# Kernel optimization log

Hardware: AMD Instinct MI355X
Metric: run time of the kernel (lower is better)

## Reference

```python
import jax, jax.numpy as jnp
import numpy as np

E4M3_MAX = 448.0  # max finite value of float8_e4m3fn
TILE = 64


def tile_quant_dequant(x):
    # per-row 1x64 tile quantization: scale = amax(tile)/448, fp8 e4m3 round-trip
    M, K = x.shape
    xt = x.reshape(M, K // TILE, TILE)
    amax = jnp.max(jnp.abs(xt), axis=-1, keepdims=True)
    scale = jnp.maximum(amax, 1e-12) / E4M3_MAX
    q = (xt / scale).astype(jnp.float8_e4m3fn).astype(jnp.float32)
    return (q * scale).reshape(M, K)


def block_quant_dequant(w):
    # 64x64 block quantization of the weight matrix
    N, K = w.shape
    wb = w.reshape(N // TILE, TILE, K // TILE, TILE)
    amax = jnp.max(jnp.abs(wb), axis=(1, 3), keepdims=True)
    scale = jnp.maximum(amax, 1e-12) / E4M3_MAX
    q = (wb / scale).astype(jnp.float8_e4m3fn).astype(jnp.float32)
    return (q * scale).reshape(N, K)


def setup_inputs() -> dict:
    key = jax.random.key(0)
    k1, k2 = jax.random.split(key)
    B, S, K, N = 2, 4096, 4096, 4096
    x = jax.random.normal(k1, (B, S, K), dtype=jnp.float32)
    # kaiming_uniform_(a=sqrt(5)) on [N,K] -> U(-1/sqrt(K), 1/sqrt(K))
    bound = float(1.0 / np.sqrt(K))
    weight = jax.random.uniform(k2, (N, K), jnp.float32, -bound, bound)
    bias = jnp.zeros((N,), jnp.float32)
    return {"x": x, "weight": weight, "bias": bias}


def reference(x, weight, bias):
    N, K = weight.shape
    x2d = x.reshape(-1, K)                     # [M, K]
    xq = tile_quant_dequant(x2d)               # simulated fp8 tile-quantized input
    wq = block_quant_dequant(weight)           # simulated fp8 block-quantized weight
    # fp8 GEMM with scales == matmul of dequantized operands (fp32 accumulation),
    # low-precision output then fp32 bias add (bf16 + fp32 bias -> fp32 in torch)
    out = jnp.matmul(xq, wq.T).astype(jnp.bfloat16).astype(jnp.float32)
    out = out + bias
    return out.reshape(*x.shape[:-1], N)
```

## Files before the change

### kernel.cpp

```cpp
#include <hip/hip_runtime.h>

typedef __attribute__((ext_vector_type(4))) float f32x4;
typedef __attribute__((ext_vector_type(16))) float f32x16;
typedef __attribute__((ext_vector_type(4))) int i32x4;
typedef __attribute__((ext_vector_type(8))) int i32x8;

__device__ __forceinline__ unsigned char enc_e4m3(float y) {
    unsigned int u = __float_as_uint(y);
    unsigned int s = (u >> 31) << 7;
    unsigned int a = u & 0x7fffffffu;
    if (a >= 0x3C800000u) {
        unsigned int r = a + 0x7FFFFu + ((a >> 20) & 1u);
        r &= 0xFFF00000u;
        if (r > 0x43E00000u) r = 0x43E00000u;
        unsigned int e = (r >> 23) - 120u;
        return (unsigned char)(s | (e << 3) | ((r >> 20) & 7u));
    } else {
        int m = (int)rintf(__uint_as_float(a) * 512.0f);
        return (unsigned char)(s | (unsigned)m);
    }
}

__device__ __forceinline__ unsigned short f32_to_bf16_bits(float f) {
    unsigned int u = __float_as_uint(f);
    u += 0x7FFFu + ((u >> 16) & 1u);
    return (unsigned short)(u >> 16);
}

__global__ __launch_bounds__(256) void quant_x_kernel(const float* __restrict__ x,
                                                      unsigned char* __restrict__ xq,
                                                      float* __restrict__ xsT,
                                                      long long n4, int K, int M) {
    long long g = (long long)blockIdx.x * 256 + threadIdx.x;
    if (g >= n4) return;
    f32x4 v = ((const f32x4*)x)[g];
    float a = fmaxf(fmaxf(fabsf(v.x), fabsf(v.y)), fmaxf(fabsf(v.z), fabsf(v.w)));
    a = fmaxf(a, __shfl_xor(a, 1));
    a = fmaxf(a, __shfl_xor(a, 2));
    a = fmaxf(a, __shfl_xor(a, 4));
    a = fmaxf(a, __shfl_xor(a, 8));
    float scale = fmaxf(a, 1e-12f) / 448.0f;
    long long flat = g * 4;
    uchar4 o;
    o.x = enc_e4m3(v.x / scale);
    o.y = enc_e4m3(v.y / scale);
    o.z = enc_e4m3(v.z / scale);
    o.w = enc_e4m3(v.w / scale);
    *(uchar4*)(xq + flat) = o;
    int row = (int)(flat / K);
    int rem = (int)(flat % K);
    if ((rem & 63) == 0)
        xsT[(size_t)(rem >> 6) * M + row] = scale;
}

__global__ __launch_bounds__(256) void quant_w_kernel(const float* __restrict__ w,
                                                      unsigned char* __restrict__ wq,
                                                      float* __restrict__ ws,
                                                      int N, int K) {
    const int nb = blockIdx.y, kb = blockIdx.x;
    const int KT = K >> 6;
    const int t = threadIdx.x;
    const int rgrp = t >> 4;
    const int cchk = t & 15;
    f32x4 v[4];
    float a = 0.0f;
#pragma unroll
    for (int i = 0; i < 4; ++i) {
        int row = nb * 64 + rgrp + i * 16;
        v[i] = *(const f32x4*)(w + (size_t)row * K + kb * 64 + cchk * 4);
        a = fmaxf(a, fmaxf(fmaxf(fabsf(v[i].x), fabsf(v[i].y)),
                           fmaxf(fabsf(v[i].z), fabsf(v[i].w))));
    }
#pragma unroll
    for (int off = 1; off < 64; off <<= 1) a = fmaxf(a, __shfl_xor(a, off));
    __shared__ float sm[4];
    if ((t & 63) == 0) sm[t >> 6] = a;
    __syncthreads();
    a = fmaxf(fmaxf(sm[0], sm[1]), fmaxf(sm[2], sm[3]));
    float scale = fmaxf(a, 1e-12f) / 448.0f;
#pragma unroll
    for (int i = 0; i < 4; ++i) {
        int row = nb * 64 + rgrp + i * 16;
        uchar4 o;
        o.x = enc_e4m3(v[i].x / scale);
        o.y = enc_e4m3(v[i].y / scale);
        o.z = enc_e4m3(v[i].z / scale);
        o.w = enc_e4m3(v[i].w / scale);
        *(uchar4*)(wq + (size_t)row * K + kb * 64 + cchk * 4) = o;
    }
    if (t == 0) ws[(size_t)nb * KT + kb] = scale;
}

#define GLDS(srcp, ldsp) __builtin_amdgcn_global_load_lds( \
    (__attribute__((address_space(1))) void*)(srcp),       \
    (__attribute__((address_space(3))) void*)(ldsp), 16, 0, 0)

__global__ __launch_bounds__(512, 2) void gemm_fp8(const unsigned char* __restrict__ Aq,
                                                   const unsigned char* __restrict__ Bq,
                                                   const float* __restrict__ xsT,
                                                   const float* __restrict__ wss,
                                                   const float* __restrict__ bias,
                                                   float* __restrict__ C,
                                                   int M, int N, int K) {
    __shared__ unsigned char Al[2][16384];
    __shared__ unsigned char Bl[2][16384];
    const int tid = threadIdx.x;
    const int wid = tid >> 6;
    const int lane = tid & 63;
    const int wm = wid >> 2, wn = wid & 3;
    const int l31 = lane & 31, h = lane >> 5;
    const int KT = K >> 6, NT = KT;

    const int nbx = N >> 8;
    const int nwg = (M >> 8) * nbx;
    const int bid = blockIdx.x;
    const int swz = (bid & 7) * (nwg >> 3) + (bid >> 3);
    const int tm = swz / nbx, tn = swz % nbx;

    const unsigned char* gA = Aq + (size_t)tm * 256 * K;
    const unsigned char* gB = Bq + (size_t)tn * 256 * K;

    const int gswz = (((lane & 3) ^ ((lane >> 3) & 3)) << 4);

    const int fsw = (l31 >> 1) & 3;
    const int slotLo = (2 * h) ^ fsw;
    const int oX = (wm * 128 + l31) * 64;
    const int oW = (wn * 64 + l31) * 64;
    const int oXlo = oX + slotLo * 16, oXhi = oX + (slotLo ^ 1) * 16;
    const int oWlo = oW + slotLo * 16, oWhi = oW + (slotLo ^ 1) * 16;

    const int iRow = tm * 256 + wm * 128 + l31;
    const int jbw  = tn * 4 + wn;

    const f32x16 z16 = {0.f,0.f,0.f,0.f,0.f,0.f,0.f,0.f,0.f,0.f,0.f,0.f,0.f,0.f,0.f,0.f};
    f32x16 macc[2][4];
#pragma unroll
    for (int n = 0; n < 2; ++n)
#pragma unroll
        for (int m = 0; m < 4; ++m) macc[n][m] = z16;

    i32x4 xlo[4], xhi[4], wlo[2], whi[2];
    float xsA[4], xsB[4], wsA = 0.f, wsB = 0.f, sarr[4];

    auto STG = [&](int t, int bufn) {
#pragma unroll
        for (int i = 0; i < 2; ++i) {
            int seg = wid * 2 + i;
            int row = seg * 16 + (lane >> 2);
            GLDS(gA + (size_t)row * K + (size_t)t * 64 + gswz, (char*)&Al[bufn][0] + seg * 1024);
            GLDS(gB + (size_t)row * K + (size_t)t * 64 + gswz, (char*)&Bl[bufn][0] + seg * 1024);
        }
    };

    auto RD_X = [&](int buf, int mi) {
        xlo[mi] = *(const i32x4*)(&Al[buf][oXlo + mi * 2048]);
        xhi[mi] = *(const i32x4*)(&Al[buf][oXhi + mi * 2048]);
    };
    auto RD_W = [&](int buf, int ni) {
        wlo[ni] = *(const i32x4*)(&Bl[buf][oWlo + ni * 2048]);
        whi[ni] = *(const i32x4*)(&Bl[buf][oWhi + ni * 2048]);
    };

    auto CL = [&](int ni, int mi0) {
        i32x8 wf = __builtin_shufflevector(wlo[ni], whi[ni], 0, 1, 2, 3, 4, 5, 6, 7);
#pragma unroll
        for (int q = 0; q < 2; ++q) {
            const int mi = mi0 + q;
            i32x8 xf = __builtin_shufflevector(xlo[mi], xhi[mi], 0, 1, 2, 3, 4, 5, 6, 7);
            f32x16 p = __builtin_amdgcn_mfma_scale_f32_32x32x64_f8f6f4(
                wf, xf, z16, 0, 0, 0, 0x7F7F7F7F, 0, 0x7F7F7F7F);
            macc[ni][mi] += p * sarr[mi];
        }
    };

    STG(0, 0);
#pragma unroll
    for (int m = 0; m < 4; ++m) xsA[m] = xsT[iRow + m * 32];
    wsA = wss[(size_t)jbw * KT];
    asm volatile("s_waitcnt vmcnt(0)" ::: "memory");
    asm volatile("s_barrier" ::: "memory");
    RD_W(0, 0); RD_X(0, 0); RD_X(0, 1);

    auto TILE = [&](int buf, int tnx, const float (&xsC)[4], float wsC,
                    float (&xsN)[4], float& wsN) {
        const int nb = buf ^ 1;
#pragma unroll
        for (int m = 0; m < 4; ++m) sarr[m] = xsC[m] * wsC;

        STG(tnx, nb);
#pragma unroll
        for (int m = 0; m < 4; ++m) xsN[m] = xsT[(size_t)tnx * M + iRow + m * 32];
        wsN = wss[(size_t)jbw * KT + tnx];

        RD_W(buf, 1);
        asm volatile("s_waitcnt lgkmcnt(2)" ::: "memory");
        __builtin_amdgcn_sched_barrier(0);
        __builtin_amdgcn_s_setprio(1);
        CL(0, 0);
        __builtin_amdgcn_s_setprio(0);

        RD_X(buf, 2); RD_X(buf, 3);
        asm volatile("s_waitcnt lgkmcnt(4)" ::: "memory");
        __builtin_amdgcn_sched_barrier(0);
        __builtin_amdgcn_s_setprio(1);
        CL(1, 0);
        __builtin_amdgcn_s_setprio(0);

        asm volatile("s_waitcnt lgkmcnt(0)" ::: "memory");
        __builtin_amdgcn_sched_barrier(0);
        __builtin_amdgcn_s_setprio(1);
        CL(0, 2);
        CL(1, 2);
        __builtin_amdgcn_s_setprio(0);

        asm volatile("s_waitcnt vmcnt(0)" ::: "memory");
        asm volatile("s_barrier" ::: "memory");
        RD_W(nb, 0); RD_X(nb, 0); RD_X(nb, 1);
    };

    for (int t = 0; t < NT; t += 2) {
        int t1 = t + 1;
        int t2 = (t + 2 < NT) ? (t + 2) : 0;
        TILE(0, t1, xsA, wsA, xsB, wsB);
        TILE(1, t2, xsB, wsB, xsA, wsA);
    }

    const int i0 = tm * 256 + wm * 128 + l31;
    const int jn = tn * 256 + wn * 64 + 4 * h;
#pragma unroll
    for (int ni = 0; ni < 2; ++ni) {
#pragma unroll
        for (int mi = 0; mi < 4; ++mi) {
            const int row = i0 + mi * 32;
#pragma unroll
            for (int q = 0; q < 4; ++q) {
                const int col = jn + ni * 32 + 8 * q;
                f32x4 bv = *(const f32x4*)(bias + col);
                f32x4 vo;
#pragma unroll
                for (int j = 0; j < 4; ++j) {
                    unsigned short b = f32_to_bf16_bits(macc[ni][mi][q * 4 + j]);
                    vo[j] = __uint_as_float(((unsigned int)b) << 16) + bv[j];
                }
                *(f32x4*)(C + (size_t)row * N + col) = vo;
            }
        }
    }
}

extern "C" void kernel_launch(void* const* d_in, const int* in_sizes, int n_in,
                              void* d_out, int out_size, void* d_ws, size_t ws_size,
                              hipStream_t stream) {
    const float* x    = (const float*)d_in[0];
    const float* w    = (const float*)d_in[1];
    const float* bias = (const float*)d_in[2];
    float* out = (float*)d_out;

    const int N = in_sizes[2];
    const long long KL = (long long)in_sizes[1] / N;
    const int K = (int)KL;
    const int M = (int)((long long)in_sizes[0] / KL);
    const int KT = K / 64;

    unsigned char* xq = (unsigned char*)d_ws;
    unsigned char* wq = xq + (size_t)M * K;
    float* xsT = (float*)(wq + (size_t)N * K);
    float* wss = xsT + (size_t)KT * M;

    long long n4 = (long long)M * K / 4;
    quant_x_kernel<<<(unsigned)((n4 + 255) / 256), 256, 0, stream>>>(x, xq, xsT, n4, K, M);

    dim3 gw(K / 64, N / 64);
    quant_w_kernel<<<gw, 256, 0, stream>>>(w, wq, wss, N, K);

    const int nwg = (M / 256) * (N / 256);
    gemm_fp8<<<nwg, 512, 0, stream>>>(xq, wq, xsT, wss, bias, out, M, N, K);
}
```

Baseline: 272.4 us.

## Split GEMM tile across 16 waves with 64x64 per-wave subtiles

The GEMM workgroup grows from 512 to 1024 threads while keeping the 256x256 output tile. Each wave now computes a 64x64 subtile (2x2 MFMAs) instead of 128x64, and each wave issues a single global-to-LDS copy per operand per k-step. The fine-grained interleaving of LDS reads with MFMA groups is replaced by one bulk read followed by all four MFMAs. The goal is more latency hiding through more resident waves. In exchange, LDS reads per MFMA rise and the software pipelining is lost. The launch bounds of (1024, 4) may also force a very tight register budget and cause spilling.

```diff
diff --git a/kernel.cpp b/kernel.cpp
--- a/kernel.cpp
+++ b/kernel.cpp
@@ -95,13 +95,13 @@
     (__attribute__((address_space(1))) void*)(srcp),       \
     (__attribute__((address_space(3))) void*)(ldsp), 16, 0, 0)
 
-__global__ __launch_bounds__(512, 2) void gemm_fp8(const unsigned char* __restrict__ Aq,
-                                                   const unsigned char* __restrict__ Bq,
-                                                   const float* __restrict__ xsT,
-                                                   const float* __restrict__ wss,
-                                                   const float* __restrict__ bias,
-                                                   float* __restrict__ C,
-                                                   int M, int N, int K) {
+__global__ __launch_bounds__(1024, 4) void gemm_fp8(const unsigned char* __restrict__ Aq,
+                                                    const unsigned char* __restrict__ Bq,
+                                                    const float* __restrict__ xsT,
+                                                    const float* __restrict__ wss,
+                                                    const float* __restrict__ bias,
+                                                    float* __restrict__ C,
+                                                    int M, int N, int K) {
     __shared__ unsigned char Al[2][16384];
     __shared__ unsigned char Bl[2][16384];
     const int tid = threadIdx.x;
@@ -124,98 +124,81 @@
 
     const int fsw = (l31 >> 1) & 3;
     const int slotLo = (2 * h) ^ fsw;
-    const int oX = (wm * 128 + l31) * 64;
+    const int oX = (wm * 64 + l31) * 64;
     const int oW = (wn * 64 + l31) * 64;
     const int oXlo = oX + slotLo * 16, oXhi = oX + (slotLo ^ 1) * 16;
     const int oWlo = oW + slotLo * 16, oWhi = oW + (slotLo ^ 1) * 16;
 
-    const int iRow = tm * 256 + wm * 128 + l31;
+    const int iRow = tm * 256 + wm * 64 + l31;
     const int jbw  = tn * 4 + wn;
 
     const f32x16 z16 = {0.f,0.f,0.f,0.f,0.f,0.f,0.f,0.f,0.f,0.f,0.f,0.f,0.f,0.f,0.f,0.f};
-    f32x16 macc[2][4];
+    f32x16 macc[2][2];
 #pragma unroll
     for (int n = 0; n < 2; ++n)
 #pragma unroll
-        for (int m = 0; m < 4; ++m) macc[n][m] = z16;
-
-    i32x4 xlo[4], xhi[4], wlo[2], whi[2];
-    float xsA[4], xsB[4], wsA = 0.f, wsB = 0.f, sarr[4];
+        for (int m = 0; m < 2; ++m) macc[n][m] = z16;
+
+    i32x4 xlo[2], xhi[2], wlo[2], whi[2];
+    float xsA[2], xsB[2], wsA = 0.f, wsB = 0.f, sarr[2];
 
     auto STG = [&](int t, int bufn) {
-#pragma unroll
-        for (int i = 0; i < 2; ++i) {
-            int seg = wid * 2 + i;
-            int row = seg * 16 + (lane >> 2);
-            GLDS(gA + (size_t)row * K + (size_t)t * 64 + gswz, (char*)&Al[bufn][0] + seg * 1024);
-            GLDS(gB + (size_t)row * K + (size_t)t * 64 + gswz, (char*)&Bl[bufn][0] + seg * 1024);
-        }
+        int row = wid * 16 + (lane >> 2);
+        GLDS(gA + (size_t)row * K + (size_t)t * 64 + gswz, (char*)&Al[bufn][0] + wid * 1024);
+        GLDS(gB + (size_t)row * K + (size_t)t * 64 + gswz, (char*)&Bl[bufn][0] + wid * 1024);
     };
 
-    auto RD_X = [&](int buf, int mi) {
-        xlo[mi] = *(const i32x4*)(&Al[buf][oXlo + mi * 2048]);
-        xhi[mi] = *(const i32x4*)(&Al[buf][oXhi + mi * 2048]);
+    auto RD_ALL = [&](int buf) {
+#pragma unroll
+        for (int mi = 0; mi < 2; ++mi) {
+            xlo[mi] = *(const i32x4*)(&Al[buf][oXlo + mi * 2048]);
+            xhi[mi] = *(const i32x4*)(&Al[buf][oXhi + mi * 2048]);
+        }
+#pragma unroll
+        for (int ni = 0; ni < 2; ++ni) {
+            wlo[ni] = *(const i32x4*)(&Bl[buf][oWlo + ni * 2048]);
+            whi[ni] = *(const i32x4*)(&Bl[buf][oWhi + ni * 2048]);
+        }
     };
-    auto RD_W = [&](int buf, int ni) {
-        wlo[ni] = *(const i32x4*)(&Bl[buf][oWlo + ni * 2048]);
-        whi[ni] = *(const i32x4*)(&Bl[buf][oWhi + ni * 2048]);
-    };
-
-    auto CL = [&](int ni, int mi0) {
-        i32x8 wf = __builtin_shufflevector(wlo[ni], whi[ni], 0, 1, 2, 3, 4, 5, 6, 7);
-#pragma unroll
-        for (int q = 0; q < 2; ++q) {
-            const int mi = mi0 + q;
-            i32x8 xf = __builtin_shufflevector(xlo[mi], xhi[mi], 0, 1, 2, 3, 4, 5, 6, 7);
-            f32x16 p = __builtin_amdgcn_mfma_scale_f32_32x32x64_f8f6f4(
-                wf, xf, z16, 0, 0, 0, 0x7F7F7F7F, 0, 0x7F7F7F7F);
-            macc[ni][mi] += p * sarr[mi];
-        }
-    };
 
     STG(0, 0);
 #pragma unroll
-    for (int m = 0; m < 4; ++m) xsA[m] = xsT[iRow + m * 32];
+    for (int m = 0; m < 2; ++m) xsA[m] = xsT[iRow + m * 32];
     wsA = wss[(size_t)jbw * KT];
     asm volatile("s_waitcnt vmcnt(0)" ::: "memory");
     asm volatile("s_barrier" ::: "memory");
-    RD_W(0, 0); RD_X(0, 0); RD_X(0, 1);
-
-    auto TILE = [&](int buf, int tnx, const float (&xsC)[4], float wsC,
-                    float (&xsN)[4], float& wsN) {
+    RD_ALL(0);
+
+    auto TILE = [&](int buf, int tnx, const float (&xsC)[2], float wsC,
+                    float (&xsN)[2], float& wsN) {
         const int nb = buf ^ 1;
-#pragma unroll
-        for (int m = 0; m < 4; ++m) sarr[m] = xsC[m] * wsC;
+        sarr[0] = xsC[0] * wsC;
+        sarr[1] = xsC[1] * wsC;
 
         STG(tnx, nb);
-#pragma unroll
-        for (int m = 0; m < 4; ++m) xsN[m] = xsT[(size_t)tnx * M + iRow + m * 32];
+        xsN[0] = xsT[(size_t)tnx * M + iRow];
+        xsN[1] = xsT[(size_t)tnx * M + iRow + 32];
         wsN = wss[(size_t)jbw * KT + tnx];
-
-        RD_W(buf, 1);
-        asm volatile("s_waitcnt lgkmcnt(2)" ::: "memory");
-        __builtin_amdgcn_sched_barrier(0);
-        __builtin_amdgcn_s_setprio(1);
-        CL(0, 0);
-        __builtin_amdgcn_s_setprio(0);
-
-        RD_X(buf, 2); RD_X(buf, 3);
-        asm volatile("s_waitcnt lgkmcnt(4)" ::: "memory");
-        __builtin_amdgcn_sched_barrier(0);
-        __builtin_amdgcn_s_setprio(1);
-        CL(1, 0);
-        __builtin_amdgcn_s_setprio(0);
 
         asm volatile("s_waitcnt lgkmcnt(0)" ::: "memory");
         __builtin_amdgcn_sched_barrier(0);
         __builtin_amdgcn_s_setprio(1);
-        CL(0, 2);
-        CL(1, 2);
+#pragma unroll
+        for (int ni = 0; ni < 2; ++ni) {
+            i32x8 wf = __builtin_shufflevector(wlo[ni], whi[ni], 0, 1, 2, 3, 4, 5, 6, 7);
+#pragma unroll
+            for (int mi = 0; mi < 2; ++mi) {
+                i32x8 xf = __builtin_shufflevector(xlo[mi], xhi[mi], 0, 1, 2, 3, 4, 5, 6, 7);
+                f32x16 p = __builtin_amdgcn_mfma_scale_f32_32x32x64_f8f6f4(
+                    wf, xf, z16, 0, 0, 0, 0x7F7F7F7F, 0, 0x7F7F7F7F);
+                macc[ni][mi] += p * sarr[mi];
+            }
+        }
         __builtin_amdgcn_s_setprio(0);
 
         asm volatile("s_waitcnt vmcnt(0)" ::: "memory");
         asm volatile("s_barrier" ::: "memory");
-        RD_W(nb, 0); RD_X(nb, 0); RD_X(nb, 1);
+        RD_ALL(nb);
     };
 
     for (int t = 0; t < NT; t += 2) {
@@ -225,12 +208,12 @@
         TILE(1, t2, xsB, wsB, xsA, wsA);
     }
 
-    const int i0 = tm * 256 + wm * 128 + l31;
+    const int i0 = tm * 256 + wm * 64 + l31;
     const int jn = tn * 256 + wn * 64 + 4 * h;
 #pragma unroll
     for (int ni = 0; ni < 2; ++ni) {
 #pragma unroll
-        for (int mi = 0; mi < 4; ++mi) {
+        for (int mi = 0; mi < 2; ++mi) {
             const int row = i0 + mi * 32;
 #pragma unroll
             for (int q = 0; q < 4; ++q) {
@@ -274,5 +257,5 @@
     quant_w_kernel<<<gw, 256, 0, stream>>>(w, wq, wss, N, K);
 
     const int nwg = (M / 256) * (N / 256);
-    gemm_fp8<<<nwg, 512, 0, stream>>>(xq, wq, xsT, wss, bias, out, M, N, K);
-}
+    gemm_fp8<<<nwg, 1024, 0, stream>>>(xq, wq, xsT, wss, bias, out, M, N, K);
+}
```

Result: slower. 525.0 us (+92.7%).

## Stage two 64-wide K tiles per pipeline step to halve barriers

Applied to the files above, without the earlier changes.

Each double-buffered pipeline stage now loads and computes a 128-wide K slab, two 64-wide sub-tiles, instead of one. Shared memory per block doubles to 128 KB. The goal is to halve the number of s_barrier and vmcnt(0) sync points per K sweep. In exchange, the per-k-tile scale loads are no longer prefetched a stage ahead and are issued right before use. The larger LDS footprint likely limits residency to one workgroup per CU, despite the launch bounds asking for two.

```diff
diff --git a/kernel.cpp b/kernel.cpp
--- a/kernel.cpp
+++ b/kernel.cpp
@@ -102,14 +102,15 @@
                                                    const float* __restrict__ bias,
                                                    float* __restrict__ C,
                                                    int M, int N, int K) {
-    __shared__ unsigned char Al[2][16384];
-    __shared__ unsigned char Bl[2][16384];
+    __shared__ unsigned char Al[65536];
+    __shared__ unsigned char Bl[65536];
     const int tid = threadIdx.x;
     const int wid = tid >> 6;
     const int lane = tid & 63;
     const int wm = wid >> 2, wn = wid & 3;
     const int l31 = lane & 31, h = lane >> 5;
-    const int KT = K >> 6, NT = KT;
+    const int KT = K >> 6;
+    const int NT2 = K >> 7;
 
     const int nbx = N >> 8;
     const int nwg = (M >> 8) * nbx;
@@ -140,25 +141,27 @@
         for (int m = 0; m < 4; ++m) macc[n][m] = z16;
 
     i32x4 xlo[4], xhi[4], wlo[2], whi[2];
-    float xsA[4], xsB[4], wsA = 0.f, wsB = 0.f, sarr[4];
-
-    auto STG = [&](int t, int bufn) {
+    float sc[4];
+
+    auto STG = [&](int t64, int bufn, int half) {
 #pragma unroll
         for (int i = 0; i < 2; ++i) {
             int seg = wid * 2 + i;
             int row = seg * 16 + (lane >> 2);
-            GLDS(gA + (size_t)row * K + (size_t)t * 64 + gswz, (char*)&Al[bufn][0] + seg * 1024);
-            GLDS(gB + (size_t)row * K + (size_t)t * 64 + gswz, (char*)&Bl[bufn][0] + seg * 1024);
-        }
-    };
-
-    auto RD_X = [&](int buf, int mi) {
-        xlo[mi] = *(const i32x4*)(&Al[buf][oXlo + mi * 2048]);
-        xhi[mi] = *(const i32x4*)(&Al[buf][oXhi + mi * 2048]);
-    };
-    auto RD_W = [&](int buf, int ni) {
-        wlo[ni] = *(const i32x4*)(&Bl[buf][oWlo + ni * 2048]);
-        whi[ni] = *(const i32x4*)(&Bl[buf][oWhi + ni * 2048]);
+            size_t go = (size_t)row * K + (size_t)t64 * 64 + gswz;
+            int db = bufn * 32768 + half * 16384 + seg * 1024;
+            GLDS(gA + go, (char*)&Al[0] + db);
+            GLDS(gB + go, (char*)&Bl[0] + db);
+        }
+    };
+
+    auto RD_X = [&](const unsigned char* p, int mi) {
+        xlo[mi] = *(const i32x4*)(p + oXlo + mi * 2048);
+        xhi[mi] = *(const i32x4*)(p + oXhi + mi * 2048);
+    };
+    auto RD_W = [&](const unsigned char* p, int ni) {
+        wlo[ni] = *(const i32x4*)(p + oWlo + ni * 2048);
+        whi[ni] = *(const i32x4*)(p + oWhi + ni * 2048);
     };
 
     auto CL = [&](int ni, int mi0) {
@@ -169,60 +172,76 @@
             i32x8 xf = __builtin_shufflevector(xlo[mi], xhi[mi], 0, 1, 2, 3, 4, 5, 6, 7);
             f32x16 p = __builtin_amdgcn_mfma_scale_f32_32x32x64_f8f6f4(
                 wf, xf, z16, 0, 0, 0, 0x7F7F7F7F, 0, 0x7F7F7F7F);
-            macc[ni][mi] += p * sarr[mi];
-        }
-    };
-
-    STG(0, 0);
-#pragma unroll
-    for (int m = 0; m < 4; ++m) xsA[m] = xsT[iRow + m * 32];
-    wsA = wss[(size_t)jbw * KT];
+            macc[ni][mi] += p * sc[mi];
+        }
+    };
+
+    STG(0, 0, 0);
+    STG(1, 0, 1);
     asm volatile("s_waitcnt vmcnt(0)" ::: "memory");
     asm volatile("s_barrier" ::: "memory");
-    RD_W(0, 0); RD_X(0, 0); RD_X(0, 1);
-
-    auto TILE = [&](int buf, int tnx, const float (&xsC)[4], float wsC,
-                    float (&xsN)[4], float& wsN) {
+    RD_W(&Bl[0], 0); RD_X(&Al[0], 0); RD_X(&Al[0], 1);
+
+    auto TILE = [&](int buf, int Tc, int Tn) {
         const int nb = buf ^ 1;
-#pragma unroll
-        for (int m = 0; m < 4; ++m) sarr[m] = xsC[m] * wsC;
-
-        STG(tnx, nb);
-#pragma unroll
-        for (int m = 0; m < 4; ++m) xsN[m] = xsT[(size_t)tnx * M + iRow + m * 32];
-        wsN = wss[(size_t)jbw * KT + tnx];
-
-        RD_W(buf, 1);
+        const unsigned char* pX0 = &Al[0] + buf * 32768;
+        const unsigned char* pX1 = pX0 + 16384;
+        const unsigned char* pW0 = &Bl[0] + buf * 32768;
+        const unsigned char* pW1 = pW0 + 16384;
+        const unsigned char* pXn = &Al[0] + nb * 32768;
+        const unsigned char* pWn = &Bl[0] + nb * 32768;
+
+        float ws0 = wss[(size_t)jbw * KT + 2 * Tc];
+        float ws1 = wss[(size_t)jbw * KT + 2 * Tc + 1];
+        float xs1v[4];
+#pragma unroll
+        for (int m = 0; m < 4; ++m) {
+            sc[m]   = xsT[(size_t)(2 * Tc) * M + iRow + m * 32] * ws0;
+            xs1v[m] = xsT[(size_t)(2 * Tc + 1) * M + iRow + m * 32] * ws1;
+        }
+
+        STG(2 * Tn,     nb, 0);
+        STG(2 * Tn + 1, nb, 1);
+
+        RD_W(pW0, 1);
         asm volatile("s_waitcnt lgkmcnt(2)" ::: "memory");
         __builtin_amdgcn_sched_barrier(0);
-        __builtin_amdgcn_s_setprio(1);
-        CL(0, 0);
-        __builtin_amdgcn_s_setprio(0);
-
-        RD_X(buf, 2); RD_X(buf, 3);
+        __builtin_amdgcn_s_setprio(1); CL(0, 0); __builtin_amdgcn_s_setprio(0);
+
+        RD_X(pX0, 2); RD_X(pX0, 3);
         asm volatile("s_waitcnt lgkmcnt(4)" ::: "memory");
         __builtin_amdgcn_sched_barrier(0);
-        __builtin_amdgcn_s_setprio(1);
-        CL(1, 0);
-        __builtin_amdgcn_s_setprio(0);
+        __builtin_amdgcn_s_setprio(1); CL(1, 0); __builtin_amdgcn_s_setprio(0);
+
+        RD_X(pX1, 0); RD_X(pX1, 1);
+        asm volatile("s_waitcnt lgkmcnt(4)" ::: "memory");
+        __builtin_amdgcn_sched_barrier(0);
+        __builtin_amdgcn_s_setprio(1); CL(0, 2); CL(1, 2); __builtin_amdgcn_s_setprio(0);
+
+#pragma unroll
+        for (int m = 0; m < 4; ++m) sc[m] = xs1v[m];
+        RD_W(pW1, 0); RD_W(pW1, 1);
+        asm volatile("s_waitcnt lgkmcnt(2)" ::: "memory");
+        __builtin_amdgcn_sched_barrier(0);
+        __builtin_amdgcn_s_setprio(1); CL(0, 0); __builtin_amdgcn_s_setprio(0);
+
+        RD_X(pX1, 2); RD_X(pX1, 3);
+        asm volatile("s_waitcnt lgkmcnt(4)" ::: "memory");
+        __builtin_amdgcn_sched_barrier(0);
+        __builtin_amdgcn_s_setprio(1); CL(1, 0); __builtin_amdgcn_s_setprio(0);
 
         asm volatile("s_waitcnt lgkmcnt(0)" ::: "memory");
         __builtin_amdgcn_sched_barrier(0);
-        __builtin_amdgcn_s_setprio(1);
-        CL(0, 2);
-        CL(1, 2);
-        __builtin_amdgcn_s_setprio(0);
+        __builtin_amdgcn_s_setprio(1); CL(0, 2); CL(1, 2); __builtin_amdgcn_s_setprio(0);
 
         asm volatile("s_waitcnt vmcnt(0)" ::: "memory");
         asm volatile("s_barrier" ::: "memory");
-        RD_W(nb, 0); RD_X(nb, 0); RD_X(nb, 1);
-    };
-
-    for (int t = 0; t < NT; t += 2) {
-        int t1 = t + 1;
-        int t2 = (t + 2 < NT) ? (t + 2) : 0;
-        TILE(0, t1, xsA, wsA, xsB, wsB);
-        TILE(1, t2, xsB, wsB, xsA, wsA);
+        RD_W(pWn, 0); RD_X(pXn, 0); RD_X(pXn, 1);
+    };
+
+    for (int T = 0; T < NT2; T += 2) {
+        TILE(0, T, T + 1);
+        TILE(1, T + 1, (T + 2 < NT2) ? (T + 2) : 0);
     }
 
     const int i0 = tm * 256 + wm * 128 + l31;
```

After: 442.6 us. 1.62x slower.

## Preload per-tile activation and weight scales into LDS before the K loop

Applied to the files above, without the earlier changes.

Before the main loop, each workgroup copies every activation tile scale for its 256 rows and every weight block scale for its 4 column blocks into shared memory. Each iteration then reads its scale from LDS instead of issuing scattered global loads that sat inside the vmcnt(0) wait. The two-tile unrolled loop with ping-pong scale registers becomes a single loop that indexes the buffers dynamically. The cost is about 64 KB of extra LDS, roughly 129 KB per workgroup in total. That likely allows only one 512-thread workgroup per CU instead of the two requested by launch_bounds, and it adds a serial preload prologue.

```diff
diff --git a/kernel.cpp b/kernel.cpp
--- a/kernel.cpp
+++ b/kernel.cpp
@@ -102,8 +102,10 @@
                                                    const float* __restrict__ bias,
                                                    float* __restrict__ C,
                                                    int M, int N, int K) {
-    __shared__ unsigned char Al[2][16384];
-    __shared__ unsigned char Bl[2][16384];
+    __shared__ unsigned char Al[32768];
+    __shared__ unsigned char Bl[32768];
+    __shared__ float xs_l[64 * 256];
+    __shared__ float ws_l[4 * 64];
     const int tid = threadIdx.x;
     const int wid = tid >> 6;
     const int lane = tid & 63;
@@ -129,8 +131,7 @@
     const int oXlo = oX + slotLo * 16, oXhi = oX + (slotLo ^ 1) * 16;
     const int oWlo = oW + slotLo * 16, oWhi = oW + (slotLo ^ 1) * 16;
 
-    const int iRow = tm * 256 + wm * 128 + l31;
-    const int jbw  = tn * 4 + wn;
+    const int xsoff = wm * 128 + l31;
 
     const f32x16 z16 = {0.f,0.f,0.f,0.f,0.f,0.f,0.f,0.f,0.f,0.f,0.f,0.f,0.f,0.f,0.f,0.f};
     f32x16 macc[2][4];
@@ -139,90 +140,88 @@
 #pragma unroll
         for (int m = 0; m < 4; ++m) macc[n][m] = z16;
 
-    i32x4 xlo[4], xhi[4], wlo[2], whi[2];
-    float xsA[4], xsB[4], wsA = 0.f, wsB = 0.f, sarr[4];
-
-    auto STG = [&](int t, int bufn) {
+    i32x8 xf[4], wf[2];
+    float xsr[4], wsr = 0.f, scl[4];
+
+    auto STG = [&](int t64, int bufn) {
 #pragma unroll
         for (int i = 0; i < 2; ++i) {
             int seg = wid * 2 + i;
             int row = seg * 16 + (lane >> 2);
-            GLDS(gA + (size_t)row * K + (size_t)t * 64 + gswz, (char*)&Al[bufn][0] + seg * 1024);
-            GLDS(gB + (size_t)row * K + (size_t)t * 64 + gswz, (char*)&Bl[bufn][0] + seg * 1024);
+            size_t go = (size_t)row * K + (size_t)t64 * 64 + gswz;
+            GLDS(gA + go, (char*)Al + bufn * 16384 + seg * 1024);
+            GLDS(gB + go, (char*)Bl + bufn * 16384 + seg * 1024);
         }
     };
 
-    auto RD_X = [&](int buf, int mi) {
-        xlo[mi] = *(const i32x4*)(&Al[buf][oXlo + mi * 2048]);
-        xhi[mi] = *(const i32x4*)(&Al[buf][oXhi + mi * 2048]);
-    };
-    auto RD_W = [&](int buf, int ni) {
-        wlo[ni] = *(const i32x4*)(&Bl[buf][oWlo + ni * 2048]);
-        whi[ni] = *(const i32x4*)(&Bl[buf][oWhi + ni * 2048]);
+    auto RD_S = [&](int t) {
+#pragma unroll
+        for (int m = 0; m < 4; ++m) xsr[m] = xs_l[t * 256 + xsoff + m * 32];
+        wsr = ws_l[wn * KT + t];
+    };
+
+    auto RD_X = [&](const unsigned char* p, int mi) {
+        ((i32x4*)&xf[mi])[0] = *(const i32x4*)(p + oXlo + mi * 2048);
+        ((i32x4*)&xf[mi])[1] = *(const i32x4*)(p + oXhi + mi * 2048);
+    };
+    auto RD_W = [&](const unsigned char* p, int ni) {
+        ((i32x4*)&wf[ni])[0] = *(const i32x4*)(p + oWlo + ni * 2048);
+        ((i32x4*)&wf[ni])[1] = *(const i32x4*)(p + oWhi + ni * 2048);
     };
 
     auto CL = [&](int ni, int mi0) {
-        i32x8 wf = __builtin_shufflevector(wlo[ni], whi[ni], 0, 1, 2, 3, 4, 5, 6, 7);
 #pragma unroll
         for (int q = 0; q < 2; ++q) {
             const int mi = mi0 + q;
-            i32x8 xf = __builtin_shufflevector(xlo[mi], xhi[mi], 0, 1, 2, 3, 4, 5, 6, 7);
             f32x16 p = __builtin_amdgcn_mfma_scale_f32_32x32x64_f8f6f4(
-                wf, xf, z16, 0, 0, 0, 0x7F7F7F7F, 0, 0x7F7F7F7F);
-            macc[ni][mi] += p * sarr[mi];
+                wf[ni], xf[mi], z16, 0, 0, 0, 0x7F7F7F7F, 0, 0x7F7F7F7F);
+            macc[ni][mi] += p * scl[mi];
         }
     };
 
+    const int xtot = KT * 256;
+    for (int idx = tid; idx < xtot; idx += 512)
+        xs_l[idx] = xsT[(size_t)(idx >> 8) * M + tm * 256 + (idx & 255)];
+    for (int idx = tid; idx < 4 * KT; idx += 512)
+        ws_l[idx] = wss[(size_t)(tn * 4 + idx / KT) * KT + (idx % KT)];
     STG(0, 0);
-#pragma unroll
-    for (int m = 0; m < 4; ++m) xsA[m] = xsT[iRow + m * 32];
-    wsA = wss[(size_t)jbw * KT];
-    asm volatile("s_waitcnt vmcnt(0)" ::: "memory");
-    asm volatile("s_barrier" ::: "memory");
-    RD_W(0, 0); RD_X(0, 0); RD_X(0, 1);
-
-    auto TILE = [&](int buf, int tnx, const float (&xsC)[4], float wsC,
-                    float (&xsN)[4], float& wsN) {
-        const int nb = buf ^ 1;
-#pragma unroll
-        for (int m = 0; m < 4; ++m) sarr[m] = xsC[m] * wsC;
-
-        STG(tnx, nb);
-#pragma unroll
-        for (int m = 0; m < 4; ++m) xsN[m] = xsT[(size_t)tnx * M + iRow + m * 32];
-        wsN = wss[(size_t)jbw * KT + tnx];
-
-        RD_W(buf, 1);
+    __syncthreads();
+    RD_S(0);
+    __builtin_amdgcn_sched_barrier(0);
+    RD_W(Bl, 0); RD_X(Al, 0); RD_X(Al, 1);
+
+    for (int t = 0; t < NT; ++t) {
+        const int buf = t & 1;
+        const unsigned char* pX = Al + buf * 16384;
+        const unsigned char* pW = Bl + buf * 16384;
+        const unsigned char* pXn = Al + (buf ^ 1) * 16384;
+        const unsigned char* pWn = Bl + (buf ^ 1) * 16384;
+        int t1 = t + 1; if (t1 == NT) t1 = 0;
+
+#pragma unroll
+        for (int m = 0; m < 4; ++m) scl[m] = xsr[m] * wsr;
+
+        STG(t1, buf ^ 1);
+
+        RD_W(pW, 1);
         asm volatile("s_waitcnt lgkmcnt(2)" ::: "memory");
         __builtin_amdgcn_sched_barrier(0);
-        __builtin_amdgcn_s_setprio(1);
-        CL(0, 0);
-        __builtin_amdgcn_s_setprio(0);
-
-        RD_X(buf, 2); RD_X(buf, 3);
+        __builtin_amdgcn_s_setprio(1); CL(0, 0); __builtin_amdgcn_s_setprio(0);
+
+        RD_X(pX, 2); RD_X(pX, 3);
         asm volatile("s_waitcnt lgkmcnt(4)" ::: "memory");
         __builtin_amdgcn_sched_barrier(0);
-        __builtin_amdgcn_s_setprio(1);
-        CL(1, 0);
-        __builtin_amdgcn_s_setprio(0);
+        __builtin_amdgcn_s_setprio(1); CL(1, 0); __builtin_amdgcn_s_setprio(0);
 
         asm volatile("s_waitcnt lgkmcnt(0)" ::: "memory");
         __builtin_amdgcn_sched_barrier(0);
-        __builtin_amdgcn_s_setprio(1);
-        CL(0, 2);
-        CL(1, 2);
-        __builtin_amdgcn_s_setprio(0);
+        __builtin_amdgcn_s_setprio(1); CL(0, 2); CL(1, 2); __builtin_amdgcn_s_setprio(0);
 
         asm volatile("s_waitcnt vmcnt(0)" ::: "memory");
         asm volatile("s_barrier" ::: "memory");
-        RD_W(nb, 0); RD_X(nb, 0); RD_X(nb, 1);
-    };
-
-    for (int t = 0; t < NT; t += 2) {
-        int t1 = t + 1;
-        int t2 = (t + 2 < NT) ? (t + 2) : 0;
-        TILE(0, t1, xsA, wsA, xsB, wsB);
-        TILE(1, t2, xsB, wsB, xsA, wsA);
+        RD_S(t1);
+        __builtin_amdgcn_sched_barrier(0);
+        RD_W(pWn, 0); RD_X(pXn, 0); RD_X(pXn, 1);
     }
 
     const int i0 = tm * 256 + wm * 128 + l31;
```

Result: faster. 266.0 us (-2.4%).
